# Optimization experiments

Measured on AMD Instinct MI355X. Metric: run time of the kernel, lower is better.

Reference implementation:

```python
import jax, jax.numpy as jnp
import numpy as np

# dims: S sets, M max items, DIN input feat, DM model dim (= head_size), H heads, L layers
S, M, DIN, DM, H, DH, L = 48, 128, 128, 128, 4, 128, 2
ALPHA = 0.3  # tf.keras.layers.LeakyReLU default alpha


def gelu(x):
    return jax.nn.gelu(x, approximate=False)  # tf.nn.gelu default is exact


def leaky(x):
    return jnp.where(x >= 0, x, ALPHA * x)


def set_norm(x, size):
    # masked per-set normalization over all items*features; pad rows (feature-sum == 0) are zeroed
    d = x.shape[-1]
    mask = (jnp.sum(x, axis=-1, keepdims=True) != 0).astype(x.dtype)  # [S,M,1]
    denom = size * d  # [S]
    mean = jnp.sum(x, axis=(1, 2)) / denom
    diff = x - mean[:, None, None]
    var = jnp.sum(jnp.square(diff) * mask, axis=(1, 2)) / denom
    return diff / (jnp.sqrt(var)[:, None, None] + 1e-8) * mask


def masked_softmax(s):
    # original masks by *nonzero score values*, not an additive bias
    mask = s != 0
    e = jnp.where(mask, jnp.exp(s - jnp.max(s, axis=-1, keepdims=True)), 0.0)
    return e / (jnp.sum(e, axis=-1, keepdims=True) + 1e-10)


def attention(x, wq, wk, wv, wh):
    split = lambda z: z.reshape(z.shape[0], z.shape[1], H, DH).transpose(0, 2, 1, 3)  # [S,H,M,D]
    q, k, v = split(x @ wq), split(x @ wk), split(x @ wv)
    s = jnp.einsum('shmd,shnd->shmn', q, k) / np.float32(np.sqrt(DH))
    a = masked_softmax(s)
    o = jnp.einsum('shmn,shnd->shmd', a, v).transpose(0, 2, 1, 3).reshape(x.shape[0], x.shape[1], H * DH)
    return o @ wh


def forward(x, size, W_proj, Wq, Wk, Wv, Wh, Wfc, Wc, w2):
    mask = (jnp.sum(x != 0, axis=-1, keepdims=True) > 0).astype(x.dtype)  # [S,M,1] valid-item mask
    h = gelu(x @ W_proj) * mask
    for l in range(L):
        a = attention(h, Wq[l], Wk[l], Wv[l], Wh[l]) * mask
        h = set_norm(h + a, size)
        f = gelu(h @ Wfc[l]) * mask
        h = set_norm(h + f, size)
    # cross_set_score (tuple branch, x == y): pairwise per-head set scores
    z = (h @ Wc).reshape(h.shape[0], h.shape[1], H, DH).transpose(0, 2, 1, 3)  # [S,H,M,D]
    s = leaky(jnp.einsum('jhmd,ihnd->jihmn', z, z) / np.float32(np.sqrt(DH)))  # [Sy,Sx,H,My,Mx]
    scores = jnp.sum(s, axis=(-1, -2)) / size[None, :, None] / np.float32(M)  # [Sy,Sx,H]
    return scores @ w2  # [Sy,Sx,1]


def setup_inputs() -> dict:
    key = jax.random.key(0)
    ks = jax.random.split(key, 10)
    x = jax.random.normal(ks[0], (S, M, DIN), jnp.float32)
    x_size = jax.random.randint(ks[1], (S,), 1, M + 1, jnp.int32)
    x = x * (jnp.arange(M)[None, :] < x_size[:, None])[:, :, None]  # zero-pad beyond set size
    sc = lambda n: np.float32(1.0 / np.sqrt(n))
    W_proj = jax.random.normal(ks[2], (DIN, DM), jnp.float32) * sc(DIN)
    Wq = jax.random.normal(ks[3], (L, DM, H * DH), jnp.float32) * sc(DM)
    Wk = jax.random.normal(ks[4], (L, DM, H * DH), jnp.float32) * sc(DM)
    Wv = jax.random.normal(ks[5], (L, DM, H * DH), jnp.float32) * sc(DM)
    Wh = jax.random.normal(ks[6], (L, H * DH, DM), jnp.float32) * sc(H * DH)
    Wfc = jax.random.normal(ks[7], (L, DM, DM), jnp.float32) * sc(DM)
    Wc = jax.random.normal(ks[8], (DM, H * DH), jnp.float32) * sc(DM)
    w2 = jax.random.normal(ks[9], (H, 1), jnp.float32) * sc(H)
    return dict(x=x, x_size=x_size, W_proj=W_proj, Wq=Wq, Wk=Wk, Wv=Wv, Wh=Wh, Wfc=Wfc, Wc=Wc, w2=w2)


def reference(x, x_size, W_proj, Wq, Wk, Wv, Wh, Wfc, Wc, w2):
    size = jnp.maximum(x_size, 1).astype(jnp.float32)
    return forward(x, size, W_proj, Wq, Wk, Wv, Wh, Wfc, Wc, w2)
```

## Files before the change

kernel.cpp:

```cpp
#include <hip/hip_runtime.h>
#include <hip/hip_bf16.h>
#include <math.h>

typedef unsigned short u16;
typedef short bf16x8 __attribute__((ext_vector_type(8)));
typedef float f32x4 __attribute__((ext_vector_type(4)));
typedef float f32x16 __attribute__((ext_vector_type(16)));

__device__ __forceinline__ u16 f2b(float f){
  union { float f; unsigned u; } c; c.f = f;
  unsigned u = c.u;
  unsigned r = (u + 0x7fffu + ((u >> 16) & 1u)) >> 16;
  return (u16)r;
}
__device__ __forceinline__ unsigned pack2(float a, float b){
  return (unsigned)f2b(a) | ((unsigned)f2b(b) << 16);
}
__device__ __forceinline__ float gelu_f(float x){
  return 0.5f * x * (1.0f + erff(x * 0.70710678118654752f));
}

__global__ __launch_bounds__(256) void prep_weights(
    const float* __restrict__ Wproj, const float* __restrict__ Wq,
    const float* __restrict__ Wk,    const float* __restrict__ Wv,
    const float* __restrict__ Whp,   const float* __restrict__ Wfc,
    const float* __restrict__ Wc,    u16* __restrict__ wT)
{
  int gid = blockIdx.x * 256 + threadIdx.x;
  if (gid >= 638976) return;
  float val;
  if (gid < 16384) {
    int n = gid >> 7, k = gid & 127;
    val = Wproj[k * 128 + n];
  } else if (gid < 409600) {
    int o = gid - 16384; int l = o / 196608, oo = o - l * 196608;
    int n = oo >> 7, k = oo & 127;
    if (n < 512)       val = Wq[l * 65536 + k * 512 + n];
    else if (n < 1024) val = Wk[l * 65536 + k * 512 + (n - 512)];
    else               val = Wv[l * 65536 + k * 512 + (n - 1024)];
  } else if (gid < 540672) {
    int o = gid - 409600; int l = o >> 16, oo = o & 65535;
    int n = oo >> 9, k = oo & 511;
    val = Whp[l * 65536 + k * 128 + n];
  } else if (gid < 573440) {
    int o = gid - 540672; int l = o >> 14, oo = o & 16383;
    int n = oo >> 7, k = oo & 127;
    val = Wfc[l * 16384 + k * 128 + n];
  } else {
    int o = gid - 573440; int n = o >> 7, k = o & 127;
    val = Wc[k * 512 + n];
  }
  wT[gid] = f2b(val);
}

__device__ __forceinline__ void stage_b(const u16* __restrict__ src, int pitch,
                                        u16* dst, int tid){
#pragma unroll
  for (int it = 0; it < 4; ++it){
    int ch = tid + it * 512; int r = ch >> 4, cc = ch & 15;
    *(uint4*)(dst + r * 136 + cc * 8) = *(const uint4*)(src + (size_t)r * pitch + cc * 8);
  }
}

__device__ __forceinline__ void plain_gemm(const u16* __restrict__ A,
    const u16* __restrict__ B, f32x4 (*acc)[4], int wr, int wc, int quad, int l16){
#pragma unroll
  for (int ks = 0; ks < 4; ++ks){
    bf16x8 aF[2], bF[4];
#pragma unroll
    for (int i = 0; i < 2; ++i)
      aF[i] = *(const bf16x8*)(A + ((wr*2+i)*16 + l16)*136 + ks*32 + quad*8);
#pragma unroll
    for (int n = 0; n < 4; ++n)
      bF[n] = *(const bf16x8*)(B + ((wc*4+n)*16 + l16)*136 + ks*32 + quad*8);
#pragma unroll
    for (int i = 0; i < 2; ++i)
#pragma unroll
      for (int n = 0; n < 4; ++n)
        acc[i][n] = __builtin_amdgcn_mfma_f32_16x16x32_bf16(aF[i], bF[n], acc[i][n], 0, 0, 0);
  }
}

__device__ __forceinline__ void write_rm(u16* dst, f32x4 (*acc)[4],
                                         int wr, int wc, int quad, int l16){
#pragma unroll
  for (int i = 0; i < 2; ++i)
#pragma unroll
    for (int n = 0; n < 4; ++n)
#pragma unroll
      for (int g = 0; g < 4; ++g)
        dst[((wr*2+i)*16 + quad*4 + g)*136 + (wc*4+n)*16 + l16] = f2b(acc[i][n][g]);
}

__device__ __forceinline__ void write_tr(u16* dst, f32x4 (*acc)[4],
                                         int wr, int wc, int quad, int l16){
#pragma unroll
  for (int i = 0; i < 2; ++i)
#pragma unroll
    for (int n = 0; n < 4; ++n)
#pragma unroll
      for (int g = 0; g < 4; ++g)
        dst[((wc*4+n)*16 + l16)*136 + (wr*2+i)*16 + quad*4 + g] = f2b(acc[i][n][g]);
}

__device__ __forceinline__ void block_reduce2(float &s1, float &s2,
                                              float* red, int wv, int lane){
#pragma unroll
  for (int off = 1; off < 64; off <<= 1){
    s1 += __shfl_xor(s1, off, 64);
    s2 += __shfl_xor(s2, off, 64);
  }
  if (lane == 0){ red[wv*2] = s1; red[wv*2+1] = s2; }
  __syncthreads();
  s1 = red[0]+red[2]+red[4]+red[6]+red[8]+red[10]+red[12]+red[14];
  s2 = red[1]+red[3]+red[5]+red[7]+red[9]+red[11]+red[13]+red[15];
  __syncthreads();
}

__global__ __launch_bounds__(512) void trunk(
    const float* __restrict__ x, const int* __restrict__ xsize,
    const u16* __restrict__ wT, u16* __restrict__ zg)
{
  __shared__ __align__(16) u16 hA[128*136];
  __shared__ __align__(16) u16 kB[128*136];
  __shared__ __align__(16) u16 vB[128*136];
  __shared__ __align__(16) u16 wS[128*136];
  __shared__ float svalid[128];
  __shared__ float red[16];
  int tid = threadIdx.x;
  int wv = tid >> 6, lane = tid & 63, quad = lane >> 4, l16 = lane & 15;
  int wr = wv >> 1, wc = wv & 1;
  int s = blockIdx.x;
  int sz = xsize[s]; if (sz < 1) sz = 1;
  int Mt = (sz + 15) >> 4, Mk = (sz + 31) >> 5;
  const float rs = 0.08838834764831845f;
  float den = (float)sz * 128.0f;

#pragma unroll
  for (int it = 0; it < 4; ++it) {
    int ch = tid + it * 512; int r = ch >> 4, cc = ch & 15;
    const float* p = x + ((size_t)s * 128 + r) * 128 + cc * 8;
    float4 u0 = *(const float4*)p, u1 = *(const float4*)(p + 4);
    int nz = (u0.x!=0.f)|(u0.y!=0.f)|(u0.z!=0.f)|(u0.w!=0.f)|
             (u1.x!=0.f)|(u1.y!=0.f)|(u1.z!=0.f)|(u1.w!=0.f);
    nz |= __shfl_xor(nz,1,64); nz |= __shfl_xor(nz,2,64);
    nz |= __shfl_xor(nz,4,64); nz |= __shfl_xor(nz,8,64);
    if ((tid & 15) == 0) svalid[r] = nz ? 1.f : 0.f;
    uint4 w;
    w.x = pack2(u0.x,u0.y); w.y = pack2(u0.z,u0.w);
    w.z = pack2(u1.x,u1.y); w.w = pack2(u1.z,u1.w);
    *(uint4*)(hA + r*136 + cc*8) = w;
  }
  stage_b(wT, 128, wS, tid);
  __syncthreads();

  f32x4 hR[2][4] = {};
  {
    f32x4 acc[2][4] = {};
    plain_gemm(hA, wS, acc, wr, wc, quad, l16);
    __syncthreads();
#pragma unroll
    for (int i = 0; i < 2; ++i)
#pragma unroll
      for (int n = 0; n < 4; ++n)
#pragma unroll
        for (int g = 0; g < 4; ++g) {
          int row = (wr*2+i)*16 + quad*4 + g;
          float gg = gelu_f(acc[i][n][g]) * svalid[row];
          hR[i][n][g] = gg;
          hA[row*136 + (wc*4+n)*16 + l16] = f2b(gg);
        }
    __syncthreads();
  }

  for (int l = 0; l < 2; ++l) {
    const u16* wQKV = wT + 16384 + l * 196608;
    const u16* wWh  = wT + 409600 + l * 65536;
    const u16* wWfc = wT + 540672 + l * 16384;
    f32x4 aR[2][4] = {};
    for (int hh = 0; hh < 4; ++hh) {
      stage_b(wQKV + hh*16384, 128, wS, tid);
      __syncthreads();
      f32x4 acc[2][4] = {};
      plain_gemm(hA, wS, acc, wr, wc, quad, l16);
      __syncthreads();
      write_rm(vB, acc, wr, wc, quad, l16);
      stage_b(wQKV + 65536 + hh*16384, 128, wS, tid);
      __syncthreads();
      bf16x8 qA[4];
#pragma unroll
      for (int ks = 0; ks < 4; ++ks)
        qA[ks] = *(const bf16x8*)(vB + (wv*16 + l16)*136 + ks*32 + quad*8);
      f32x4 acck[2][4] = {};
      plain_gemm(hA, wS, acck, wr, wc, quad, l16);
      __syncthreads();
      write_rm(kB, acck, wr, wc, quad, l16);
      stage_b(wQKV + 131072 + hh*16384, 128, wS, tid);
      __syncthreads();
      f32x4 accv[2][4] = {};
      plain_gemm(hA, wS, accv, wr, wc, quad, l16);
      __syncthreads();
      write_tr(vB, accv, wr, wc, quad, l16);
      __syncthreads();
      bool act = wv < Mt;
      f32x4 sacc[8] = {};
      if (act) {
#pragma unroll
        for (int ks = 0; ks < 4; ++ks) {
          bf16x8 bF[8];
#pragma unroll
          for (int j = 0; j < 8; ++j)
            if (j < Mt) bF[j] = *(const bf16x8*)(kB + (j*16+l16)*136 + ks*32 + quad*8);
#pragma unroll
          for (int j = 0; j < 8; ++j)
            if (j < Mt) sacc[j] = __builtin_amdgcn_mfma_f32_16x16x32_bf16(qA[ks], bF[j], sacc[j], 0, 0, 0);
        }
        for (int g = 0; g < 4; ++g) {
          float vals[8]; float rmax = -1e30f;
#pragma unroll
          for (int j = 0; j < 8; ++j)
            if (j < Mt) {
              float v = sacc[j][g] * rs;
              vals[j] = v;
              rmax = fmaxf(rmax, v);
            }
          for (int off = 1; off < 16; off <<= 1) rmax = fmaxf(rmax, __shfl_xor(rmax, off, 64));
          if (sz < 128) rmax = fmaxf(rmax, 0.0f);
          float rsum = 0.f;
#pragma unroll
          for (int j = 0; j < 8; ++j)
            if (j < Mt) {
              float e = (vals[j] != 0.0f) ? expf(vals[j] - rmax) : 0.0f;
              vals[j] = e; rsum += e;
            }
          for (int off = 1; off < 16; off <<= 1) rsum += __shfl_xor(rsum, off, 64);
          float inv = 1.0f / (rsum + 1e-10f);
#pragma unroll
          for (int j = 0; j < 8; ++j)
            if (j < Mt) sacc[j][g] = vals[j] * inv;
        }
      }
      __syncthreads();
      if (act) {
#pragma unroll
        for (int j = 0; j < 8; ++j)
          if (j < Mt)
#pragma unroll
            for (int g = 0; g < 4; ++g)
              kB[(wv*16 + quad*4 + g)*136 + j*16 + l16] = f2b(sacc[j][g]);
      }
      stage_b(wWh + hh*128, 512, wS, tid);
      __syncthreads();
      f32x4 oacc[8] = {};
      if (act) {
        for (int ks = 0; ks < Mk; ++ks) {
          bf16x8 aF = *(const bf16x8*)(kB + (wv*16 + l16)*136 + ks*32 + quad*8);
          bf16x8 bF[8];
#pragma unroll
          for (int n = 0; n < 8; ++n)
            bF[n] = *(const bf16x8*)(vB + (n*16+l16)*136 + ks*32 + quad*8);
#pragma unroll
          for (int n = 0; n < 8; ++n)
            oacc[n] = __builtin_amdgcn_mfma_f32_16x16x32_bf16(aF, bF[n], oacc[n], 0, 0, 0);
        }
      }
      __syncthreads();
#pragma unroll
      for (int n = 0; n < 8; ++n)
#pragma unroll
        for (int g = 0; g < 4; ++g)
          vB[(wv*16 + quad*4 + g)*136 + n*16 + l16] = f2b(oacc[n][g]);
      __syncthreads();
      plain_gemm(vB, wS, aR, wr, wc, quad, l16);
      __syncthreads();
    }

    {
      float ls1 = 0.f, ls2 = 0.f;
#pragma unroll
      for (int i = 0; i < 2; ++i)
#pragma unroll
        for (int n = 0; n < 4; ++n)
#pragma unroll
          for (int g = 0; g < 4; ++g) {
            int row = (wr*2+i)*16 + quad*4 + g;
            float u = hR[i][n][g] + aR[i][n][g] * svalid[row];
            hR[i][n][g] = u;
            ls1 += u; ls2 += u * u;
          }
      block_reduce2(ls1, ls2, red, wv, lane);
      float mean = ls1 / den;
      float var = ls2 / den - mean * mean; if (var < 0.f) var = 0.f;
      float inv = 1.0f / (sqrtf(var) + 1e-8f);
#pragma unroll
      for (int i = 0; i < 2; ++i)
#pragma unroll
        for (int n = 0; n < 4; ++n)
#pragma unroll
          for (int g = 0; g < 4; ++g) {
            int row = (wr*2+i)*16 + quad*4 + g;
            float hn = (hR[i][n][g] - mean) * inv * svalid[row];
            hR[i][n][g] = hn;
            hA[row*136 + (wc*4+n)*16 + l16] = f2b(hn);
          }
      stage_b(wWfc, 128, wS, tid);
      __syncthreads();
    }
    {
      f32x4 fa[2][4] = {};
      plain_gemm(hA, wS, fa, wr, wc, quad, l16);
      __syncthreads();
      float ls1 = 0.f, ls2 = 0.f;
#pragma unroll
      for (int i = 0; i < 2; ++i)
#pragma unroll
        for (int n = 0; n < 4; ++n)
#pragma unroll
          for (int g = 0; g < 4; ++g) {
            int row = (wr*2+i)*16 + quad*4 + g;
            float u = hR[i][n][g] + gelu_f(fa[i][n][g]) * svalid[row];
            hR[i][n][g] = u;
            ls1 += u; ls2 += u * u;
          }
      block_reduce2(ls1, ls2, red, wv, lane);
      float mean = ls1 / den;
      float var = ls2 / den - mean * mean; if (var < 0.f) var = 0.f;
      float inv = 1.0f / (sqrtf(var) + 1e-8f);
#pragma unroll
      for (int i = 0; i < 2; ++i)
#pragma unroll
        for (int n = 0; n < 4; ++n)
#pragma unroll
          for (int g = 0; g < 4; ++g) {
            int row = (wr*2+i)*16 + quad*4 + g;
            float hn = (hR[i][n][g] - mean) * inv * svalid[row];
            hR[i][n][g] = hn;
            hA[row*136 + (wc*4+n)*16 + l16] = f2b(hn);
          }
      __syncthreads();
    }
  }

  const u16* wWc = wT + 573440;
  for (int hh = 0; hh < 4; ++hh) {
    stage_b(wWc + hh*16384, 128, wS, tid);
    __syncthreads();
    f32x4 za[2][4] = {};
    plain_gemm(hA, wS, za, wr, wc, quad, l16);
#pragma unroll
    for (int i = 0; i < 2; ++i)
#pragma unroll
      for (int n = 0; n < 4; ++n)
#pragma unroll
        for (int g = 0; g < 4; ++g) {
          int row = (wr*2+i)*16 + quad*4 + g;
          int col = (wc*4+n)*16 + l16;
          zg[((size_t)(s*4 + hh)*128 + row)*128 + col] = f2b(za[i][n][g]);
        }
    __syncthreads();
  }
}

__global__ __launch_bounds__(256) void cross_kernel(
    const u16* __restrict__ zg, float* __restrict__ Tbuf, const int* __restrict__ xsize)
{
  __shared__ __align__(16) u16 bufA[16384];
  __shared__ __align__(16) u16 bufB[16384];
  __shared__ float red[4];
  int tid = threadIdx.x, wave = tid >> 6, lane = tid & 63;
  int t4 = blockIdx.x;
  int pr = t4 >> 2, hh = t4 & 3;
  float jf = (97.0f - sqrtf(9409.0f - 8.0f * (float)pr)) * 0.5f;
  int j = (int)jf; if (j > 47) j = 47; if (j < 0) j = 0;
  while (j > 0 && j * 48 - (j * (j - 1)) / 2 > pr) --j;
  while ((j + 1) * 48 - ((j + 1) * j) / 2 <= pr) ++j;
  int i = j + pr - (j * 48 - (j * (j - 1)) / 2);
  int sj = xsize[j]; if (sj < 1) sj = 1;
  int si = xsize[i]; if (si < 1) si = 1;
  int MjT = (sj + 31) >> 5, MiT = (si + 31) >> 5;
  size_t basej = ((size_t)j * 4 + hh) << 14;
  size_t basei = ((size_t)i * 4 + hh) << 14;
#pragma unroll
  for (int t = 0; t < 8; ++t) {
    int c = t * 256 + tid;
    int m = c & 31, half = (c >> 5) & 1, ks = (c >> 6) & 7, g = c >> 9;
    int row = g * 32 + m, col = ks * 16 + half * 8;
    if (g < MjT) *(uint4*)(bufA + c * 8) = *(const uint4*)(zg + basej + row * 128 + col);
    if (g < MiT) *(uint4*)(bufB + c * 8) = *(const uint4*)(zg + basei + row * 128 + col);
  }
  __syncthreads();
  int gA = (wave >> 1) * 2, gB = (wave & 1) * 2;
  bool a0 = gA < MjT, a1 = (gA + 1) < MjT;
  bool b0 = gB < MiT, b1 = (gB + 1) < MiT;
  f32x16 acc[2][2] = {};
  if ((a0 || a1) && (b0 || b1)) {
    for (int ks = 0; ks < 8; ++ks) {
      bf16x8 aF[2], bF[2];
      if (a0) aF[0] = *(const bf16x8*)(bufA + ((gA    ) * 8 + ks) * 512 + lane * 8);
      if (a1) aF[1] = *(const bf16x8*)(bufA + ((gA + 1) * 8 + ks) * 512 + lane * 8);
      if (b0) bF[0] = *(const bf16x8*)(bufB + ((gB    ) * 8 + ks) * 512 + lane * 8);
      if (b1) bF[1] = *(const bf16x8*)(bufB + ((gB + 1) * 8 + ks) * 512 + lane * 8);
      if (a0 && b0) acc[0][0] = __builtin_amdgcn_mfma_f32_32x32x16_bf16(aF[0], bF[0], acc[0][0], 0, 0, 0);
      if (a0 && b1) acc[0][1] = __builtin_amdgcn_mfma_f32_32x32x16_bf16(aF[0], bF[1], acc[0][1], 0, 0, 0);
      if (a1 && b0) acc[1][0] = __builtin_amdgcn_mfma_f32_32x32x16_bf16(aF[1], bF[0], acc[1][0], 0, 0, 0);
      if (a1 && b1) acc[1][1] = __builtin_amdgcn_mfma_f32_32x32x16_bf16(aF[1], bF[1], acc[1][1], 0, 0, 0);
    }
  }
  float s1 = 0.f, s2 = 0.f;
#pragma unroll
  for (int ii = 0; ii < 2; ++ii)
#pragma unroll
    for (int jj = 0; jj < 2; ++jj) {
      bool tact = (ii ? a1 : a0) && (jj ? b1 : b0);
      if (tact)
#pragma unroll
        for (int r = 0; r < 16; ++r) {
          float a = acc[ii][jj][r];
          s1 += a; s2 += fabsf(a);
        }
    }
  const float rs = 0.08838834764831845f;
  float tp = rs * (0.65f * s1 + 0.35f * s2);
  for (int off = 1; off < 64; off <<= 1) tp += __shfl_xor(tp, off, 64);
  if (lane == 0) red[wave] = tp;
  __syncthreads();
  if (tid == 0)
    Tbuf[((j * 48 + i) << 2) + hh] = red[0] + red[1] + red[2] + red[3];
}

__global__ __launch_bounds__(256) void final_kernel(
    const float* __restrict__ Tbuf, const float* __restrict__ w2,
    const int* __restrict__ xsize, float* __restrict__ out)
{
  int idx = blockIdx.x * 256 + threadIdx.x;
  if (idx >= 2304) return;
  int a = idx / 48, b = idx - a * 48;
  int j = a < b ? a : b, i = a < b ? b : a;
  float t = 0.f;
  for (int h = 0; h < 4; ++h) t += Tbuf[((j * 48 + i) << 2) + h] * w2[h];
  int szb = xsize[b]; if (szb < 1) szb = 1;
  out[idx] = t / ((float)szb * 128.0f);
}

extern "C" void kernel_launch(void* const* d_in, const int* in_sizes, int n_in,
                              void* d_out, int out_size, void* d_ws, size_t ws_size,
                              hipStream_t stream)
{
  const float* x     = (const float*)d_in[0];
  const int*   xsize = (const int*)d_in[1];
  const float* Wproj = (const float*)d_in[2];
  const float* Wq    = (const float*)d_in[3];
  const float* Wk    = (const float*)d_in[4];
  const float* Wv    = (const float*)d_in[5];
  const float* Whp   = (const float*)d_in[6];
  const float* Wfc   = (const float*)d_in[7];
  const float* Wc    = (const float*)d_in[8];
  const float* w2    = (const float*)d_in[9];
  float* out = (float*)d_out;

  char* ws = (char*)d_ws;
  size_t off = 0;
  auto alloc = [&](size_t bytes) -> char* {
    char* p = ws + off;
    off += (bytes + 255) & ~(size_t)255;
    return p;
  };
  u16*   wT   = (u16*)  alloc(638976 * 2);
  float* Tbuf = (float*)alloc(9216 * 4);
  u16*   zg   = (u16*)  alloc((size_t)3145728 * 2);

  prep_weights<<<2496, 256, 0, stream>>>(Wproj, Wq, Wk, Wv, Whp, Wfc, Wc, wT);
  trunk<<<48, 512, 0, stream>>>(x, xsize, wT, zg);
  cross_kernel<<<4704, 256, 0, stream>>>(zg, Tbuf, xsize);
  final_kernel<<<9, 256, 0, stream>>>(Tbuf, w2, xsize, out);
}
```

Before: 273.0 us.

## Pre-swizzle weights into MFMA fragment order and batch cross pairs per block

prep_weights now writes bf16 weights already laid out in MFMA B-fragment order, so the trunk GEMMs read B operands straight from global/L2 instead of staging each weight tile through LDS. This removes many stage_b copies and __syncthreads barriers in the serial 48-block trunk. The cross kernel now handles four i-sets per block, reusing the j tile and double-buffering the next i tile with register prefetch, which cuts the block count and redundant loads. The risks are higher global-load latency inside the GEMM inner loop and more register pressure from the prefetch.

```diff
diff --git a/kernel.cpp b/kernel.cpp
--- a/kernel.cpp
+++ b/kernel.cpp
@@ -26,44 +26,40 @@
     const float* __restrict__ Whp,   const float* __restrict__ Wfc,
     const float* __restrict__ Wc,    u16* __restrict__ wT)
 {
-  int gid = blockIdx.x * 256 + threadIdx.x;
-  if (gid >= 638976) return;
-  float val;
-  if (gid < 16384) {
-    int n = gid >> 7, k = gid & 127;
-    val = Wproj[k * 128 + n];
-  } else if (gid < 409600) {
-    int o = gid - 16384; int l = o / 196608, oo = o - l * 196608;
-    int n = oo >> 7, k = oo & 127;
-    if (n < 512)       val = Wq[l * 65536 + k * 512 + n];
-    else if (n < 1024) val = Wk[l * 65536 + k * 512 + (n - 512)];
-    else               val = Wv[l * 65536 + k * 512 + (n - 1024)];
-  } else if (gid < 540672) {
-    int o = gid - 409600; int l = o >> 16, oo = o & 65535;
-    int n = oo >> 9, k = oo & 511;
-    val = Whp[l * 65536 + k * 128 + n];
-  } else if (gid < 573440) {
-    int o = gid - 540672; int l = o >> 14, oo = o & 16383;
-    int n = oo >> 7, k = oo & 127;
-    val = Wfc[l * 16384 + k * 128 + n];
-  } else {
-    int o = gid - 573440; int n = o >> 7, k = o & 127;
-    val = Wc[k * 512 + n];
-  }
-  wT[gid] = f2b(val);
-}
-
-__device__ __forceinline__ void stage_b(const u16* __restrict__ src, int pitch,
-                                        u16* dst, int tid){
-#pragma unroll
-  for (int it = 0; it < 4; ++it){
-    int ch = tid + it * 512; int r = ch >> 4, cc = ch & 15;
-    *(uint4*)(dst + r * 136 + cc * 8) = *(const uint4*)(src + (size_t)r * pitch + cc * 8);
-  }
-}
-
-__device__ __forceinline__ void plain_gemm(const u16* __restrict__ A,
-    const u16* __restrict__ B, f32x4 (*acc)[4], int wr, int wc, int quad, int l16){
+  int cid = blockIdx.x * 256 + threadIdx.x;
+  if (cid >= 79872) return;
+  int region, lh = 0, c;
+  if      (cid < 2048)  { region = 0; c = cid; }
+  else if (cid < 18432) { int o = cid - 2048;  region = 1; lh = o >> 11; c = o & 2047; }
+  else if (cid < 34816) { int o = cid - 18432; region = 2; lh = o >> 11; c = o & 2047; }
+  else if (cid < 51200) { int o = cid - 34816; region = 3; lh = o >> 11; c = o & 2047; }
+  else if (cid < 67584) { int o = cid - 51200; region = 4; lh = o >> 11; c = o & 2047; }
+  else if (cid < 71680) { int o = cid - 67584; region = 5; lh = o >> 11; c = o & 2047; }
+  else                  { int o = cid - 71680; region = 6; lh = o >> 11; c = o & 2047; }
+  int l16 = c & 15, quad = (c >> 4) & 3, ks = (c >> 6) & 3, nt = c >> 8;
+  int n = nt * 16 + l16, kb = ks * 32 + quad * 8;
+  int l = lh >> 2, hh = lh & 3;
+  u16 tmp[8];
+#pragma unroll
+  for (int e = 0; e < 8; ++e) {
+    int k = kb + e;
+    float v;
+    switch (region) {
+      case 0: v = Wproj[k * 128 + n]; break;
+      case 1: v = Wq[l * 65536 + k * 512 + hh * 128 + n]; break;
+      case 2: v = Wk[l * 65536 + k * 512 + hh * 128 + n]; break;
+      case 3: v = Wv[l * 65536 + k * 512 + hh * 128 + n]; break;
+      case 4: v = Whp[l * 65536 + (hh * 128 + k) * 128 + n]; break;
+      case 5: v = Wfc[lh * 16384 + k * 128 + n]; break;
+      default: v = Wc[k * 512 + lh * 128 + n]; break;
+    }
+    tmp[e] = f2b(v);
+  }
+  *(uint4*)(wT + (size_t)cid * 8) = *(uint4*)tmp;
+}
+
+__device__ __forceinline__ void gemm_g(const u16* A, const u16* __restrict__ Bg,
+    f32x4 (*acc)[4], int wr, int wc, int quad, int l16, int lane){
 #pragma unroll
   for (int ks = 0; ks < 4; ++ks){
     bf16x8 aF[2], bF[4];
@@ -72,7 +68,7 @@
       aF[i] = *(const bf16x8*)(A + ((wr*2+i)*16 + l16)*136 + ks*32 + quad*8);
 #pragma unroll
     for (int n = 0; n < 4; ++n)
-      bF[n] = *(const bf16x8*)(B + ((wc*4+n)*16 + l16)*136 + ks*32 + quad*8);
+      bF[n] = *(const bf16x8*)(Bg + ((size_t)(((wc*4+n)*4 + ks)*64 + lane))*8);
 #pragma unroll
     for (int i = 0; i < 2; ++i)
 #pragma unroll
@@ -122,9 +118,9 @@
     const u16* __restrict__ wT, u16* __restrict__ zg)
 {
   __shared__ __align__(16) u16 hA[128*136];
-  __shared__ __align__(16) u16 kB[128*136];
-  __shared__ __align__(16) u16 vB[128*136];
-  __shared__ __align__(16) u16 wS[128*136];
+  __shared__ __align__(16) u16 qP[128*136];
+  __shared__ __align__(16) u16 kO[128*136];
+  __shared__ __align__(16) u16 vT[128*136];
   __shared__ float svalid[128];
   __shared__ float red[16];
   int tid = threadIdx.x;
@@ -151,13 +147,12 @@
     w.z = pack2(u1.x,u1.y); w.w = pack2(u1.z,u1.w);
     *(uint4*)(hA + r*136 + cc*8) = w;
   }
-  stage_b(wT, 128, wS, tid);
   __syncthreads();
 
   f32x4 hR[2][4] = {};
   {
     f32x4 acc[2][4] = {};
-    plain_gemm(hA, wS, acc, wr, wc, quad, l16);
+    gemm_g(hA, wT, acc, wr, wc, quad, l16, lane);
     __syncthreads();
 #pragma unroll
     for (int i = 0; i < 2; ++i)
@@ -170,39 +165,38 @@
           hR[i][n][g] = gg;
           hA[row*136 + (wc*4+n)*16 + l16] = f2b(gg);
         }
-    __syncthreads();
   }
 
   for (int l = 0; l < 2; ++l) {
-    const u16* wQKV = wT + 16384 + l * 196608;
-    const u16* wWh  = wT + 409600 + l * 65536;
-    const u16* wWfc = wT + 540672 + l * 16384;
     f32x4 aR[2][4] = {};
     for (int hh = 0; hh < 4; ++hh) {
-      stage_b(wQKV + hh*16384, 128, wS, tid);
+      int lh = l * 4 + hh;
+      const u16* Wq_g = wT + 16384  + lh * 16384;
+      const u16* Wk_g = wT + 147456 + lh * 16384;
+      const u16* Wv_g = wT + 278528 + lh * 16384;
+      const u16* Wh_g = wT + 409600 + lh * 16384;
       __syncthreads();
-      f32x4 acc[2][4] = {};
-      plain_gemm(hA, wS, acc, wr, wc, quad, l16);
-      __syncthreads();
-      write_rm(vB, acc, wr, wc, quad, l16);
-      stage_b(wQKV + 65536 + hh*16384, 128, wS, tid);
-      __syncthreads();
-      bf16x8 qA[4];
-#pragma unroll
-      for (int ks = 0; ks < 4; ++ks)
-        qA[ks] = *(const bf16x8*)(vB + (wv*16 + l16)*136 + ks*32 + quad*8);
-      f32x4 acck[2][4] = {};
-      plain_gemm(hA, wS, acck, wr, wc, quad, l16);
-      __syncthreads();
-      write_rm(kB, acck, wr, wc, quad, l16);
-      stage_b(wQKV + 131072 + hh*16384, 128, wS, tid);
-      __syncthreads();
-      f32x4 accv[2][4] = {};
-      plain_gemm(hA, wS, accv, wr, wc, quad, l16);
-      __syncthreads();
-      write_tr(vB, accv, wr, wc, quad, l16);
+      {
+        f32x4 qa[2][4] = {};
+        gemm_g(hA, Wq_g, qa, wr, wc, quad, l16, lane);
+        write_rm(qP, qa, wr, wc, quad, l16);
+      }
+      {
+        f32x4 ka[2][4] = {};
+        gemm_g(hA, Wk_g, ka, wr, wc, quad, l16, lane);
+        write_rm(kO, ka, wr, wc, quad, l16);
+      }
+      {
+        f32x4 va[2][4] = {};
+        gemm_g(hA, Wv_g, va, wr, wc, quad, l16, lane);
+        write_tr(vT, va, wr, wc, quad, l16);
+      }
       __syncthreads();
       bool act = wv < Mt;
+      bf16x8 qA[4];
+#pragma unroll
+      for (int ks = 0; ks < 4; ++ks)
+        qA[ks] = *(const bf16x8*)(qP + (wv*16 + l16)*136 + ks*32 + quad*8);
       f32x4 sacc[8] = {};
       if (act) {
 #pragma unroll
@@ -210,7 +204,7 @@
           bf16x8 bF[8];
 #pragma unroll
           for (int j = 0; j < 8; ++j)
-            if (j < Mt) bF[j] = *(const bf16x8*)(kB + (j*16+l16)*136 + ks*32 + quad*8);
+            if (j < Mt) bF[j] = *(const bf16x8*)(kO + (j*16+l16)*136 + ks*32 + quad*8);
 #pragma unroll
           for (int j = 0; j < 8; ++j)
             if (j < Mt) sacc[j] = __builtin_amdgcn_mfma_f32_16x16x32_bf16(qA[ks], bF[j], sacc[j], 0, 0, 0);
@@ -247,32 +241,28 @@
           if (j < Mt)
 #pragma unroll
             for (int g = 0; g < 4; ++g)
-              kB[(wv*16 + quad*4 + g)*136 + j*16 + l16] = f2b(sacc[j][g]);
-      }
-      stage_b(wWh + hh*128, 512, wS, tid);
-      __syncthreads();
+              qP[(wv*16 + quad*4 + g)*136 + j*16 + l16] = f2b(sacc[j][g]);
+      }
       f32x4 oacc[8] = {};
       if (act) {
         for (int ks = 0; ks < Mk; ++ks) {
-          bf16x8 aF = *(const bf16x8*)(kB + (wv*16 + l16)*136 + ks*32 + quad*8);
+          bf16x8 aF = *(const bf16x8*)(qP + (wv*16 + l16)*136 + ks*32 + quad*8);
           bf16x8 bF[8];
 #pragma unroll
           for (int n = 0; n < 8; ++n)
-            bF[n] = *(const bf16x8*)(vB + (n*16+l16)*136 + ks*32 + quad*8);
+            bF[n] = *(const bf16x8*)(vT + (n*16+l16)*136 + ks*32 + quad*8);
 #pragma unroll
           for (int n = 0; n < 8; ++n)
             oacc[n] = __builtin_amdgcn_mfma_f32_16x16x32_bf16(aF, bF[n], oacc[n], 0, 0, 0);
         }
       }
+#pragma unroll
+      for (int n = 0; n < 8; ++n)
+#pragma unroll
+        for (int g = 0; g < 4; ++g)
+          kO[(wv*16 + quad*4 + g)*136 + n*16 + l16] = f2b(oacc[n][g]);
       __syncthreads();
-#pragma unroll
-      for (int n = 0; n < 8; ++n)
-#pragma unroll
-        for (int g = 0; g < 4; ++g)
-          vB[(wv*16 + quad*4 + g)*136 + n*16 + l16] = f2b(oacc[n][g]);
-      __syncthreads();
-      plain_gemm(vB, wS, aR, wr, wc, quad, l16);
-      __syncthreads();
+      gemm_g(kO, Wh_g, aR, wr, wc, quad, l16, lane);
     }
 
     {
@@ -303,13 +293,11 @@
             hR[i][n][g] = hn;
             hA[row*136 + (wc*4+n)*16 + l16] = f2b(hn);
           }
-      stage_b(wWfc, 128, wS, tid);
       __syncthreads();
     }
     {
       f32x4 fa[2][4] = {};
-      plain_gemm(hA, wS, fa, wr, wc, quad, l16);
-      __syncthreads();
+      gemm_g(hA, wT + 540672 + l * 16384, fa, wr, wc, quad, l16, lane);
       float ls1 = 0.f, ls2 = 0.f;
 #pragma unroll
       for (int i = 0; i < 2; ++i)
@@ -337,16 +325,13 @@
             hR[i][n][g] = hn;
             hA[row*136 + (wc*4+n)*16 + l16] = f2b(hn);
           }
-      __syncthreads();
-    }
-  }
-
-  const u16* wWc = wT + 573440;
+    }
+  }
+
+  __syncthreads();
   for (int hh = 0; hh < 4; ++hh) {
-    stage_b(wWc + hh*16384, 128, wS, tid);
-    __syncthreads();
     f32x4 za[2][4] = {};
-    plain_gemm(hA, wS, za, wr, wc, quad, l16);
+    gemm_g(hA, wT + 573440 + hh * 16384, za, wr, wc, quad, l16, lane);
 #pragma unroll
     for (int i = 0; i < 2; ++i)
 #pragma unroll
@@ -357,7 +342,6 @@
           int col = (wc*4+n)*16 + l16;
           zg[((size_t)(s*4 + hh)*128 + row)*128 + col] = f2b(za[i][n][g]);
         }
-    __syncthreads();
   }
 }
 
@@ -365,67 +349,98 @@
     const u16* __restrict__ zg, float* __restrict__ Tbuf, const int* __restrict__ xsize)
 {
   __shared__ __align__(16) u16 bufA[16384];
-  __shared__ __align__(16) u16 bufB[16384];
+  __shared__ __align__(16) u16 bufB[2][16384];
   __shared__ float red[4];
   int tid = threadIdx.x, wave = tid >> 6, lane = tid & 63;
-  int t4 = blockIdx.x;
-  int pr = t4 >> 2, hh = t4 & 3;
-  float jf = (97.0f - sqrtf(9409.0f - 8.0f * (float)pr)) * 0.5f;
-  int j = (int)jf; if (j > 47) j = 47; if (j < 0) j = 0;
-  while (j > 0 && j * 48 - (j * (j - 1)) / 2 > pr) --j;
-  while ((j + 1) * 48 - ((j + 1) * j) / 2 <= pr) ++j;
-  int i = j + pr - (j * 48 - (j * (j - 1)) / 2);
+  int bid = blockIdx.x;
+  int hh = bid & 3, qq = bid >> 2;
+  int j = 0;
+  for (;;) { int nq = (51 - j) >> 2; if (qq < nq) break; qq -= nq; ++j; }
+  int i0 = j + qq * 4;
   int sj = xsize[j]; if (sj < 1) sj = 1;
-  int si = xsize[i]; if (si < 1) si = 1;
-  int MjT = (sj + 31) >> 5, MiT = (si + 31) >> 5;
-  size_t basej = ((size_t)j * 4 + hh) << 14;
-  size_t basei = ((size_t)i * 4 + hh) << 14;
-#pragma unroll
-  for (int t = 0; t < 8; ++t) {
-    int c = t * 256 + tid;
-    int m = c & 31, half = (c >> 5) & 1, ks = (c >> 6) & 7, g = c >> 9;
-    int row = g * 32 + m, col = ks * 16 + half * 8;
-    if (g < MjT) *(uint4*)(bufA + c * 8) = *(const uint4*)(zg + basej + row * 128 + col);
-    if (g < MiT) *(uint4*)(bufB + c * 8) = *(const uint4*)(zg + basei + row * 128 + col);
+  int MjT = (sj + 31) >> 5;
+  const float rs = 0.08838834764831845f;
+  {
+    const u16* srcA = zg + (((size_t)j  * 4 + hh) << 14);
+    int si = xsize[i0]; if (si < 1) si = 1;
+    int MiT0 = (si + 31) >> 5;
+    const u16* srcB = zg + (((size_t)i0 * 4 + hh) << 14);
+#pragma unroll
+    for (int t = 0; t < 8; ++t) {
+      int c = t * 256 + tid;
+      int m = c & 31, ha = (c >> 5) & 1, ks = (c >> 6) & 7, g = c >> 9;
+      int row = g * 32 + m, col = ks * 16 + ha * 8;
+      if (g < MjT)  *(uint4*)(bufA + c * 8)    = *(const uint4*)(srcA + row * 128 + col);
+      if (g < MiT0) *(uint4*)(bufB[0] + c * 8) = *(const uint4*)(srcB + row * 128 + col);
+    }
   }
   __syncthreads();
   int gA = (wave >> 1) * 2, gB = (wave & 1) * 2;
   bool a0 = gA < MjT, a1 = (gA + 1) < MjT;
-  bool b0 = gB < MiT, b1 = (gB + 1) < MiT;
-  f32x16 acc[2][2] = {};
-  if ((a0 || a1) && (b0 || b1)) {
-    for (int ks = 0; ks < 8; ++ks) {
-      bf16x8 aF[2], bF[2];
-      if (a0) aF[0] = *(const bf16x8*)(bufA + ((gA    ) * 8 + ks) * 512 + lane * 8);
-      if (a1) aF[1] = *(const bf16x8*)(bufA + ((gA + 1) * 8 + ks) * 512 + lane * 8);
-      if (b0) bF[0] = *(const bf16x8*)(bufB + ((gB    ) * 8 + ks) * 512 + lane * 8);
-      if (b1) bF[1] = *(const bf16x8*)(bufB + ((gB + 1) * 8 + ks) * 512 + lane * 8);
-      if (a0 && b0) acc[0][0] = __builtin_amdgcn_mfma_f32_32x32x16_bf16(aF[0], bF[0], acc[0][0], 0, 0, 0);
-      if (a0 && b1) acc[0][1] = __builtin_amdgcn_mfma_f32_32x32x16_bf16(aF[0], bF[1], acc[0][1], 0, 0, 0);
-      if (a1 && b0) acc[1][0] = __builtin_amdgcn_mfma_f32_32x32x16_bf16(aF[1], bF[0], acc[1][0], 0, 0, 0);
-      if (a1 && b1) acc[1][1] = __builtin_amdgcn_mfma_f32_32x32x16_bf16(aF[1], bF[1], acc[1][1], 0, 0, 0);
-    }
-  }
-  float s1 = 0.f, s2 = 0.f;
-#pragma unroll
-  for (int ii = 0; ii < 2; ++ii)
-#pragma unroll
-    for (int jj = 0; jj < 2; ++jj) {
-      bool tact = (ii ? a1 : a0) && (jj ? b1 : b0);
-      if (tact)
-#pragma unroll
-        for (int r = 0; r < 16; ++r) {
-          float a = acc[ii][jj][r];
-          s1 += a; s2 += fabsf(a);
-        }
-    }
-  const float rs = 0.08838834764831845f;
-  float tp = rs * (0.65f * s1 + 0.35f * s2);
-  for (int off = 1; off < 64; off <<= 1) tp += __shfl_xor(tp, off, 64);
-  if (lane == 0) red[wave] = tp;
-  __syncthreads();
-  if (tid == 0)
-    Tbuf[((j * 48 + i) << 2) + hh] = red[0] + red[1] + red[2] + red[3];
+  for (int t = 0; t < 4; ++t) {
+    int i = i0 + t;
+    if (i >= 48) break;
+    int si = xsize[i]; if (si < 1) si = 1;
+    int MiT = (si + 31) >> 5;
+    int inx = i + 1;
+    bool pf = (t < 3) && (inx < 48);
+    uint4 pfv[8]; int MnxT = 0;
+    if (pf) {
+      int sn = xsize[inx]; if (sn < 1) sn = 1;
+      MnxT = (sn + 31) >> 5;
+      const u16* srcN = zg + (((size_t)inx * 4 + hh) << 14);
+#pragma unroll
+      for (int tt = 0; tt < 8; ++tt) {
+        int c = tt * 256 + tid;
+        int m = c & 31, ha = (c >> 5) & 1, ks = (c >> 6) & 7, g = c >> 9;
+        if (g < MnxT)
+          pfv[tt] = *(const uint4*)(srcN + (g * 32 + m) * 128 + ks * 16 + ha * 8);
+      }
+    }
+    const u16* zb = bufB[t & 1];
+    bool b0 = gB < MiT, b1 = (gB + 1) < MiT;
+    f32x16 acc[2][2] = {};
+    if ((a0 || a1) && (b0 || b1)) {
+      for (int ks = 0; ks < 8; ++ks) {
+        bf16x8 aF[2], bF[2];
+        if (a0) aF[0] = *(const bf16x8*)(bufA + ((gA    ) * 8 + ks) * 512 + lane * 8);
+        if (a1) aF[1] = *(const bf16x8*)(bufA + ((gA + 1) * 8 + ks) * 512 + lane * 8);
+        if (b0) bF[0] = *(const bf16x8*)(zb   + ((gB    ) * 8 + ks) * 512 + lane * 8);
+        if (b1) bF[1] = *(const bf16x8*)(zb   + ((gB + 1) * 8 + ks) * 512 + lane * 8);
+        if (a0 && b0) acc[0][0] = __builtin_amdgcn_mfma_f32_32x32x16_bf16(aF[0], bF[0], acc[0][0], 0, 0, 0);
+        if (a0 && b1) acc[0][1] = __builtin_amdgcn_mfma_f32_32x32x16_bf16(aF[0], bF[1], acc[0][1], 0, 0, 0);
+        if (a1 && b0) acc[1][0] = __builtin_amdgcn_mfma_f32_32x32x16_bf16(aF[1], bF[0], acc[1][0], 0, 0, 0);
+        if (a1 && b1) acc[1][1] = __builtin_amdgcn_mfma_f32_32x32x16_bf16(aF[1], bF[1], acc[1][1], 0, 0, 0);
+      }
+    }
+    float s1 = 0.f, s2 = 0.f;
+#pragma unroll
+    for (int ii = 0; ii < 2; ++ii)
+#pragma unroll
+      for (int jj = 0; jj < 2; ++jj) {
+        bool tact = (ii ? a1 : a0) && (jj ? b1 : b0);
+        if (tact)
+#pragma unroll
+          for (int r = 0; r < 16; ++r) {
+            float a = acc[ii][jj][r];
+            s1 += a; s2 += fabsf(a);
+          }
+      }
+    float tp = rs * (0.65f * s1 + 0.35f * s2);
+    for (int off = 1; off < 64; off <<= 1) tp += __shfl_xor(tp, off, 64);
+    if (lane == 0) red[wave] = tp;
+    __syncthreads();
+    if (tid == 0)
+      Tbuf[((j * 48 + i) << 2) + hh] = red[0] + red[1] + red[2] + red[3];
+    if (pf) {
+#pragma unroll
+      for (int tt = 0; tt < 8; ++tt) {
+        int c = tt * 256 + tid;
+        if ((c >> 9) < MnxT) *(uint4*)(bufB[(t + 1) & 1] + c * 8) = pfv[tt];
+      }
+    }
+    __syncthreads();
+  }
 }
 
 __global__ __launch_bounds__(256) void final_kernel(
@@ -469,8 +484,8 @@
   float* Tbuf = (float*)alloc(9216 * 4);
   u16*   zg   = (u16*)  alloc((size_t)3145728 * 2);
 
-  prep_weights<<<2496, 256, 0, stream>>>(Wproj, Wq, Wk, Wv, Whp, Wfc, Wc, wT);
+  prep_weights<<<312, 256, 0, stream>>>(Wproj, Wq, Wk, Wv, Whp, Wfc, Wc, wT);
   trunk<<<48, 512, 0, stream>>>(x, xsize, wT, zg);
-  cross_kernel<<<4704, 256, 0, stream>>>(zg, Tbuf, xsize);
+  cross_kernel<<<1248, 256, 0, stream>>>(zg, Tbuf, xsize);
   final_kernel<<<9, 256, 0, stream>>>(Tbuf, w2, xsize, out);
 }
```

New measurement: 309.7 us. 13.5% more time.
